# Performance work log

Hardware: AMD Instinct MI355X
Metric: run time of the kernel (lower is better)

## Reference

```python
import jax, jax.numpy as jnp
import numpy as np

N = 100000
E = 1600000
D_IN = 128
D_OUT = 64


def setup_inputs() -> dict:
    key = jax.random.key(0)
    k1, k2, k3, k4, k5 = jax.random.split(key, 5)
    x = jax.random.normal(k1, (N, D_IN), dtype=jnp.float32)
    edge_row = jax.random.randint(k2, (E,), 0, N, dtype=jnp.int32)
    edge_col = jax.random.randint(k3, (E,), 0, N, dtype=jnp.int32)
    edge_val = jax.random.uniform(k4, (E,), dtype=jnp.float32)
    # Glorot-uniform init as in the torch module
    init_range = np.sqrt(6.0 / (D_IN + D_OUT))
    weight = jax.random.uniform(k5, (D_IN, D_OUT), dtype=jnp.float32,
                                minval=-init_range, maxval=init_range)
    return {"x": x, "edge_row": edge_row, "edge_col": edge_col,
            "edge_val": edge_val, "weight": weight}


def reference(x, edge_row, edge_col, edge_val, weight):
    # Dense projection: [N, D_in] @ [D_in, D_out] -> [N, D_out]
    xw = jnp.matmul(x, weight)
    # Sparse aggregation (SpMM with COO support): out[r] += val * xw[c]
    msgs = edge_val[:, None] * xw[edge_col]          # [E, D_out]
    out = jax.ops.segment_sum(msgs, edge_row, num_segments=x.shape[0])
    # bias=False, activation=relu
    return jax.nn.relu(out)
```

## Files before the change

### kernel.cpp

```cpp
#include <hip/hip_runtime.h>

#define NN 100000
#define DIN 128
#define DOUT 64
#define NE 1600000

#define BSHIFT 6
#define BROWS 64
#define NB 1563
#define CAP 1536
#define EPB 8192
#define NBLK 196

#define XWB_B  0u
#define GCUR_B 12800000u
#define BPAD_B (GCUR_B + 8192u)
#define WS_NEED (BPAD_B + (unsigned)NB * CAP * 8u)

typedef unsigned short u16;
typedef unsigned int u32;
typedef __attribute__((ext_vector_type(8))) short v8s;
typedef __attribute__((ext_vector_type(4))) float v4f;

__device__ __forceinline__ float bf2f(u16 u) {
  return __uint_as_float(((u32)u) << 16);
}
__device__ __forceinline__ u16 f2bf(float f) {
  u32 x = __float_as_uint(f);
  u32 r = x + 0x7fffu + ((x >> 16) & 1u);
  return (u16)(r >> 16);
}

__global__ __launch_bounds__(256) void gemm_kernel(
    const float* __restrict__ x, const float* __restrict__ w,
    u16* __restrict__ xwb) {
  __shared__ u16 wlds[16 * 64 * 8];
  const int t = threadIdx.x;
  const int lane = t & 63;
  const int wv = t >> 6;

  #pragma unroll
  for (int pi = 0; pi < 4; ++pi) {
    const int p = t * 4 + pi;
    const int f = p >> 6, lp = p & 63;
    const int kc = f >> 2, nc = f & 3;
    const int kg = lp >> 4, lr = lp & 15;
    const int kbase = kc * 32 + kg * 8;
    u32 pk[4];
    #pragma unroll
    for (int h = 0; h < 4; ++h) {
      const u32 lo = f2bf(w[(kbase + 2 * h)     * DOUT + nc * 16 + lr]);
      const u32 hi = f2bf(w[(kbase + 2 * h + 1) * DOUT + nc * 16 + lr]);
      pk[h] = lo | (hi << 16);
    }
    *reinterpret_cast<uint4*>(&wlds[p * 8]) =
        make_uint4(pk[0], pk[1], pk[2], pk[3]);
  }
  __syncthreads();

  const int row0 = blockIdx.x * 64 + wv * 16;
  if (row0 >= NN) return;
  const int lrow = lane & 15;
  const int lkg  = lane >> 4;

  v8s Bf[4][4];
  #pragma unroll
  for (int kc = 0; kc < 4; ++kc)
    #pragma unroll
    for (int nc = 0; nc < 4; ++nc)
      Bf[kc][nc] = *reinterpret_cast<const v8s*>(
          &wlds[((kc * 4 + nc) * 64 + lane) * 8]);

  const float* xr = x + (size_t)(row0 + lrow) * DIN + lkg * 8;
  float4 xa[4][2];
  #pragma unroll
  for (int kc = 0; kc < 4; ++kc) {
    xa[kc][0] = *reinterpret_cast<const float4*>(xr + kc * 32);
    xa[kc][1] = *reinterpret_cast<const float4*>(xr + kc * 32 + 4);
  }

  v4f acc[4];
  #pragma unroll
  for (int nc = 0; nc < 4; ++nc) acc[nc] = (v4f){0.f, 0.f, 0.f, 0.f};

  #pragma unroll
  for (int kc = 0; kc < 4; ++kc) {
    v8s Af;
    Af[0] = (short)f2bf(xa[kc][0].x);
    Af[1] = (short)f2bf(xa[kc][0].y);
    Af[2] = (short)f2bf(xa[kc][0].z);
    Af[3] = (short)f2bf(xa[kc][0].w);
    Af[4] = (short)f2bf(xa[kc][1].x);
    Af[5] = (short)f2bf(xa[kc][1].y);
    Af[6] = (short)f2bf(xa[kc][1].z);
    Af[7] = (short)f2bf(xa[kc][1].w);
    #pragma unroll
    for (int nc = 0; nc < 4; ++nc)
      acc[nc] = __builtin_amdgcn_mfma_f32_16x16x32_bf16(Af, Bf[kc][nc],
                                                        acc[nc], 0, 0, 0);
  }

  #pragma unroll
  for (int nc = 0; nc < 4; ++nc)
    #pragma unroll
    for (int j = 0; j < 4; ++j)
      xwb[(size_t)(row0 + lkg * 4 + j) * DOUT + nc * 16 + lrow] =
          f2bf(acc[nc][j]);
}

__global__ __launch_bounds__(1024) void place3_kernel(
    const int* __restrict__ erow, const int* __restrict__ ecol,
    const float* __restrict__ eval_, int* __restrict__ gcur,
    int2* __restrict__ bpad) {
  __shared__ int  hist[2048];
  __shared__ int  lofs[NB + 1];
  __shared__ int  lcur[NB];
  __shared__ int  base_[NB];
  __shared__ int  wtot[16];
  __shared__ u16  sb[EPB];
  __shared__ int2 dstl[EPB];

  const int t = threadIdx.x;
  const int lane = t & 63;
  const int wv = t >> 6;
  const int blk = blockIdx.x;
  const int e0 = blk * EPB;
  const int e1 = min(e0 + EPB, NE);
  const int ecount = e1 - e0;

  for (int i = t; i < 2048; i += 1024) hist[i] = 0;
  for (int i = t; i < NB; i += 1024) lcur[i] = 0;
  __syncthreads();

  int er[8];
  #pragma unroll
  for (int k = 0; k < 8; ++k) {
    const int e = e0 + t + k * 1024;
    er[k] = (e < e1) ? erow[e] : -1;
    if (er[k] >= 0) atomicAdd(&hist[er[k] >> BSHIFT], 1);
  }
  __syncthreads();

  const int ha = hist[2 * t], hb = hist[2 * t + 1];
  const int ps = ha + hb;
  int s = ps;
  #pragma unroll
  for (int o = 1; o < 64; o <<= 1) {
    const int u = __shfl_up(s, o);
    if (lane >= o) s += u;
  }
  if (lane == 63) wtot[wv] = s;
  __syncthreads();
  int woff = 0;
  #pragma unroll
  for (int w = 0; w < 16; ++w) woff += (w < wv) ? wtot[w] : 0;
  const int excl = woff + s - ps;
  if (2 * t     <= NB) lofs[2 * t]     = excl;
  if (2 * t + 1 <= NB) lofs[2 * t + 1] = excl + ha;
  for (int i = t; i < NB; i += 1024) {
    const int h = hist[i];
    base_[i] = h ? atomicAdd(&gcur[i], h) : 0;
  }
  __syncthreads();

  #pragma unroll
  for (int k = 0; k < 8; ++k) {
    const int e = e0 + t + k * 1024;
    if (er[k] >= 0) {
      const int b = er[k] >> BSHIFT;
      const int pos = lofs[b] + atomicAdd(&lcur[b], 1);
      int2 q;
      q.x = ((er[k] & (BROWS - 1)) << 17) | ecol[e];
      q.y = __float_as_int(eval_[e]);
      dstl[pos] = q;
      sb[pos] = (u16)b;
    }
  }
  __syncthreads();

  for (int p = t; p < ecount; p += 1024) {
    const int b = sb[p];
    const int rk = base_[b] + (p - lofs[b]);
    if (rk < CAP) bpad[(long)b * CAP + rk] = dstl[p];
  }
}

__global__ __launch_bounds__(256) void agg2_kernel(
    const int* __restrict__ gcur, const int2* __restrict__ bpad,
    const u16* __restrict__ xwb, float* __restrict__ out) {
  __shared__ int2 dst[CAP];
  __shared__ int  hist[BROWS];
  __shared__ int  lptr[BROWS + 1];
  __shared__ int  cur[BROWS];

  const int bucket = blockIdx.x;
  const int t = threadIdx.x;
  const int count = min(gcur[bucket], CAP);
  const long sbase = (long)bucket * CAP;

  if (t < BROWS) hist[t] = 0;
  __syncthreads();

  int2 qr[6];
  #pragma unroll
  for (int k = 0; k < 6; ++k) {
    const int e = t + k * 256;
    if (e < count) {
      qr[k] = bpad[sbase + e];
      atomicAdd(&hist[(qr[k].x >> 17) & (BROWS - 1)], 1);
    }
  }
  __syncthreads();

  if (t < 64) {
    const int v = hist[t];
    int s = v;
    #pragma unroll
    for (int o = 1; o < 64; o <<= 1) {
      const int u = __shfl_up(s, o);
      if (t >= o) s += u;
    }
    lptr[t + 1] = s;
    cur[t] = s - v;
    if (t == 0) lptr[0] = 0;
  }
  __syncthreads();

  #pragma unroll
  for (int k = 0; k < 6; ++k) {
    const int e = t + k * 256;
    if (e < count) {
      const int r = (qr[k].x >> 17) & (BROWS - 1);
      const int pos = atomicAdd(&cur[r], 1);
      dst[pos] = qr[k];
    }
  }
  __syncthreads();

  const int lane = t & 63;
  const int wave = t >> 6;
  const int slot = lane >> 4;
  const int li   = lane & 15;
  const int row0 = bucket << BSHIFT;
  const int cmax = count - 1;

  for (int r = wave; r < BROWS; r += 4) {
    const int row = row0 + r;
    if (row >= NN) break;
    const int s = lptr[r], en = lptr[r + 1];
    float a0 = 0.f, a1 = 0.f, a2 = 0.f, a3 = 0.f;
    for (int e = s; e < en; e += 8) {
      {
        const int idx = e + slot;
        const int2 q = dst[min(idx, cmax)];
        const float v = (idx < en) ? __int_as_float(q.y) : 0.f;
        const u32 col = (u32)q.x & 0x1FFFFu;
        const uint2 g = *reinterpret_cast<const uint2*>(
            xwb + (size_t)col * DOUT + li * 4);
        a0 = fmaf(v, __uint_as_float(g.x << 16), a0);
        a1 = fmaf(v, __uint_as_float(g.x & 0xFFFF0000u), a1);
        a2 = fmaf(v, __uint_as_float(g.y << 16), a2);
        a3 = fmaf(v, __uint_as_float(g.y & 0xFFFF0000u), a3);
      }
      {
        const int idx = e + 4 + slot;
        const int2 q = dst[min(idx, cmax)];
        const float v = (idx < en) ? __int_as_float(q.y) : 0.f;
        const u32 col = (u32)q.x & 0x1FFFFu;
        const uint2 g = *reinterpret_cast<const uint2*>(
            xwb + (size_t)col * DOUT + li * 4);
        a0 = fmaf(v, __uint_as_float(g.x << 16), a0);
        a1 = fmaf(v, __uint_as_float(g.x & 0xFFFF0000u), a1);
        a2 = fmaf(v, __uint_as_float(g.y << 16), a2);
        a3 = fmaf(v, __uint_as_float(g.y & 0xFFFF0000u), a3);
      }
    }
    a0 += __shfl_xor(a0, 16); a0 += __shfl_xor(a0, 32);
    a1 += __shfl_xor(a1, 16); a1 += __shfl_xor(a1, 32);
    a2 += __shfl_xor(a2, 16); a2 += __shfl_xor(a2, 32);
    a3 += __shfl_xor(a3, 16); a3 += __shfl_xor(a3, 32);
    if (slot == 0) {
      float4 o;
      o.x = fmaxf(a0, 0.f); o.y = fmaxf(a1, 0.f);
      o.z = fmaxf(a2, 0.f); o.w = fmaxf(a3, 0.f);
      *reinterpret_cast<float4*>(&out[(size_t)row * DOUT + li * 4]) = o;
    }
  }
}

__global__ __launch_bounds__(256) void scatter_kernel(
    const int* __restrict__ erow, const int* __restrict__ ecol,
    const float* __restrict__ eval_, const u16* __restrict__ xwb,
    float* __restrict__ out) {
  const int wave = (blockIdx.x * blockDim.x + threadIdx.x) >> 6;
  const int lane = threadIdx.x & 63;
  const int nwaves = (gridDim.x * blockDim.x) >> 6;
  const int per = (NE + nwaves - 1) / nwaves;
  const int e0 = wave * per;
  const int e1 = min(e0 + per, NE);
  for (int base = e0; base < e1; base += 64) {
    const int e = base + lane;
    int r = 0, c = 0; float v = 0.f;
    if (e < e1) { r = erow[e]; c = ecol[e]; v = eval_[e]; }
    const int cnt = min(64, e1 - base);
    for (int j = 0; j < cnt; ++j) {
      const int rj = __shfl(r, j);
      const int cj = __shfl(c, j);
      const float vj = __shfl(v, j);
      atomicAdd(&out[rj * DOUT + lane], vj * bf2f(xwb[cj * DOUT + lane]));
    }
  }
}

__global__ __launch_bounds__(256) void finish_kernel(float* __restrict__ out) {
  const int idx = (blockIdx.x * blockDim.x + threadIdx.x) * 4;
  if (idx < NN * DOUT) {
    float4 a = *reinterpret_cast<const float4*>(&out[idx]);
    a.x = fmaxf(a.x, 0.f); a.y = fmaxf(a.y, 0.f);
    a.z = fmaxf(a.z, 0.f); a.w = fmaxf(a.w, 0.f);
    *reinterpret_cast<float4*>(&out[idx]) = a;
  }
}

extern "C" void kernel_launch(void* const* d_in, const int* in_sizes, int n_in,
                              void* d_out, int out_size, void* d_ws, size_t ws_size,
                              hipStream_t stream) {
  const float* x     = (const float*)d_in[0];
  const int*   erow  = (const int*)d_in[1];
  const int*   ecol  = (const int*)d_in[2];
  const float* eval_ = (const float*)d_in[3];
  const float* w     = (const float*)d_in[4];
  float* out = (float*)d_out;

  char* ws = (char*)d_ws;
  u16* xwb = (u16*)(ws + XWB_B);

  const int gemm_grid = (NN + 63) / 64;
  gemm_kernel<<<gemm_grid, 256, 0, stream>>>(x, w, xwb);

  if (ws_size >= (size_t)WS_NEED) {
    int*  gcur = (int*)(ws + GCUR_B);
    int2* bpad = (int2*)(ws + BPAD_B);

    hipMemsetAsync(gcur, 0, NB * 4, stream);
    place3_kernel<<<NBLK, 1024, 0, stream>>>(erow, ecol, eval_, gcur, bpad);
    agg2_kernel<<<NB, 256, 0, stream>>>(gcur, bpad, xwb, out);
  } else {
    hipMemsetAsync(d_out, 0, (size_t)NN * DOUT * sizeof(float), stream);
    scatter_kernel<<<2048, 256, 0, stream>>>(erow, ecol, eval_, xwb, out);
    const int fin_grid = (NN * DOUT / 4 + 255) / 256;
    finish_kernel<<<fin_grid, 256, 0, stream>>>(out);
  }
}
```

Measured before the change: 73.89 us.

## Use 256-row buckets, fold gcur zeroing into GEMM, retune place/agg blocks

Enlarges the row buckets from 64 to 256 rows, cutting the bucket count to 391. The placement kernel now runs 512-thread blocks over 4096 edges each, and the aggregation kernel runs 512 threads per bucket with a larger LDS staging buffer. The separate memset of the bucket counters is removed; the GEMM kernel zeroes them instead, which saves one launch. Risks are lower occupancy from the larger LDS footprint (about 38KB per agg block) and bucket overflow if any bucket exceeds the 4736-edge cap.

```diff
diff --git a/kernel.cpp b/kernel.cpp
--- a/kernel.cpp
+++ b/kernel.cpp
@@ -5,17 +5,17 @@
 #define DOUT 64
 #define NE 1600000
 
-#define BSHIFT 6
-#define BROWS 64
-#define NB 1563
-#define CAP 1536
-#define EPB 8192
-#define NBLK 196
+#define BSHIFT 8
+#define BROWS 256
+#define NBB 391
+#define CAP 4736
+#define EPB 4096
+#define NBLK 391
 
 #define XWB_B  0u
 #define GCUR_B 12800000u
 #define BPAD_B (GCUR_B + 8192u)
-#define WS_NEED (BPAD_B + (unsigned)NB * CAP * 8u)
+#define WS_NEED (BPAD_B + (unsigned)NBB * CAP * 8u)
 
 typedef unsigned short u16;
 typedef unsigned int u32;
@@ -33,7 +33,10 @@
 
 __global__ __launch_bounds__(256) void gemm_kernel(
     const float* __restrict__ x, const float* __restrict__ w,
-    u16* __restrict__ xwb) {
+    u16* __restrict__ xwb, int* __restrict__ gz) {
+  if (gz != nullptr && threadIdx.x == 0 && blockIdx.x < NBB)
+    gz[blockIdx.x] = 0;
+
   __shared__ u16 wlds[16 * 64 * 8];
   const int t = threadIdx.x;
   const int lane = t & 63;
@@ -108,42 +111,47 @@
           f2bf(acc[nc][j]);
 }
 
-__global__ __launch_bounds__(1024) void place3_kernel(
+__global__ __launch_bounds__(512) void place4_kernel(
     const int* __restrict__ erow, const int* __restrict__ ecol,
     const float* __restrict__ eval_, int* __restrict__ gcur,
     int2* __restrict__ bpad) {
-  __shared__ int  hist[2048];
-  __shared__ int  lofs[NB + 1];
-  __shared__ int  lcur[NB];
-  __shared__ int  base_[NB];
-  __shared__ int  wtot[16];
+  __shared__ int  hist[512];
+  __shared__ int  lofs[512];
+  __shared__ int  lcur[512];
+  __shared__ int  base_[512];
+  __shared__ int  wtot[8];
   __shared__ u16  sb[EPB];
   __shared__ int2 dstl[EPB];
 
   const int t = threadIdx.x;
   const int lane = t & 63;
   const int wv = t >> 6;
-  const int blk = blockIdx.x;
-  const int e0 = blk * EPB;
+  const int e0 = blockIdx.x * EPB;
   const int e1 = min(e0 + EPB, NE);
   const int ecount = e1 - e0;
 
-  for (int i = t; i < 2048; i += 1024) hist[i] = 0;
-  for (int i = t; i < NB; i += 1024) lcur[i] = 0;
-  __syncthreads();
-
-  int er[8];
+  hist[t] = 0;
+  lcur[t] = 0;
+  __syncthreads();
+
+  int er[8], ec[8];
+  float ev[8];
   #pragma unroll
   for (int k = 0; k < 8; ++k) {
-    const int e = e0 + t + k * 1024;
-    er[k] = (e < e1) ? erow[e] : -1;
-    if (er[k] >= 0) atomicAdd(&hist[er[k] >> BSHIFT], 1);
-  }
-  __syncthreads();
-
-  const int ha = hist[2 * t], hb = hist[2 * t + 1];
-  const int ps = ha + hb;
-  int s = ps;
+    const int e = e0 + t + k * 512;
+    if (e < e1) {
+      er[k] = erow[e];
+      ec[k] = ecol[e];
+      ev[k] = eval_[e];
+      atomicAdd(&hist[er[k] >> BSHIFT], 1);
+    } else {
+      er[k] = -1;
+    }
+  }
+  __syncthreads();
+
+  const int h = hist[t];
+  int s = h;
   #pragma unroll
   for (int o = 1; o < 64; o <<= 1) {
     const int u = __shfl_up(s, o);
@@ -153,39 +161,31 @@
   __syncthreads();
   int woff = 0;
   #pragma unroll
-  for (int w = 0; w < 16; ++w) woff += (w < wv) ? wtot[w] : 0;
-  const int excl = woff + s - ps;
-  if (2 * t     <= NB) lofs[2 * t]     = excl;
-  if (2 * t + 1 <= NB) lofs[2 * t + 1] = excl + ha;
-  for (int i = t; i < NB; i += 1024) {
-    const int h = hist[i];
-    base_[i] = h ? atomicAdd(&gcur[i], h) : 0;
-  }
+  for (int w = 0; w < 8; ++w) woff += (w < wv) ? wtot[w] : 0;
+  lofs[t] = woff + s - h;
+  base_[t] = (h && t < NBB) ? atomicAdd(&gcur[t], h) : 0;
   __syncthreads();
 
   #pragma unroll
   for (int k = 0; k < 8; ++k) {
-    const int e = e0 + t + k * 1024;
     if (er[k] >= 0) {
       const int b = er[k] >> BSHIFT;
       const int pos = lofs[b] + atomicAdd(&lcur[b], 1);
-      int2 q;
-      q.x = ((er[k] & (BROWS - 1)) << 17) | ecol[e];
-      q.y = __float_as_int(eval_[e]);
-      dstl[pos] = q;
+      dstl[pos] = make_int2(((er[k] & (BROWS - 1)) << 17) | ec[k],
+                            __float_as_int(ev[k]));
       sb[pos] = (u16)b;
     }
   }
   __syncthreads();
 
-  for (int p = t; p < ecount; p += 1024) {
+  for (int p = t; p < ecount; p += 512) {
     const int b = sb[p];
     const int rk = base_[b] + (p - lofs[b]);
     if (rk < CAP) bpad[(long)b * CAP + rk] = dstl[p];
   }
 }
 
-__global__ __launch_bounds__(256) void agg2_kernel(
+__global__ __launch_bounds__(512) void agg5_kernel(
     const int* __restrict__ gcur, const int2* __restrict__ bpad,
     const u16* __restrict__ xwb, float* __restrict__ out) {
   __shared__ int2 dst[CAP];
@@ -201,39 +201,34 @@
   if (t < BROWS) hist[t] = 0;
   __syncthreads();
 
-  int2 qr[6];
-  #pragma unroll
-  for (int k = 0; k < 6; ++k) {
-    const int e = t + k * 256;
-    if (e < count) {
-      qr[k] = bpad[sbase + e];
-      atomicAdd(&hist[(qr[k].x >> 17) & (BROWS - 1)], 1);
-    }
-  }
+  for (int e = t; e < count; e += 512)
+    atomicAdd(&hist[(bpad[sbase + e].x >> 17) & (BROWS - 1)], 1);
   __syncthreads();
 
   if (t < 64) {
-    const int v = hist[t];
-    int s = v;
+    const int h0 = hist[4 * t],     h1 = hist[4 * t + 1];
+    const int h2 = hist[4 * t + 2], h3 = hist[4 * t + 3];
+    const int ps = h0 + h1 + h2 + h3;
+    int s = ps;
     #pragma unroll
     for (int o = 1; o < 64; o <<= 1) {
       const int u = __shfl_up(s, o);
       if (t >= o) s += u;
     }
-    lptr[t + 1] = s;
-    cur[t] = s - v;
-    if (t == 0) lptr[0] = 0;
-  }
-  __syncthreads();
-
-  #pragma unroll
-  for (int k = 0; k < 6; ++k) {
-    const int e = t + k * 256;
-    if (e < count) {
-      const int r = (qr[k].x >> 17) & (BROWS - 1);
-      const int pos = atomicAdd(&cur[r], 1);
-      dst[pos] = qr[k];
-    }
+    const int excl = s - ps;
+    lptr[4 * t]     = excl;                cur[4 * t]     = excl;
+    lptr[4 * t + 1] = excl + h0;           cur[4 * t + 1] = excl + h0;
+    lptr[4 * t + 2] = excl + h0 + h1;      cur[4 * t + 2] = excl + h0 + h1;
+    lptr[4 * t + 3] = excl + h0 + h1 + h2; cur[4 * t + 3] = excl + h0 + h1 + h2;
+    if (t == 63) lptr[BROWS] = s;
+  }
+  __syncthreads();
+
+  for (int e = t; e < count; e += 512) {
+    const int2 q = bpad[sbase + e];
+    const int r = (q.x >> 17) & (BROWS - 1);
+    const int pos = atomicAdd(&cur[r], 1);
+    dst[pos] = q;
   }
   __syncthreads();
 
@@ -244,7 +239,7 @@
   const int row0 = bucket << BSHIFT;
   const int cmax = count - 1;
 
-  for (int r = wave; r < BROWS; r += 4) {
+  for (int r = wave; r < BROWS; r += 8) {
     const int row = row0 + r;
     if (row >= NN) break;
     const int s = lptr[r], en = lptr[r + 1];
@@ -334,17 +329,16 @@
 
   char* ws = (char*)d_ws;
   u16* xwb = (u16*)(ws + XWB_B);
+  const bool big_ws = (ws_size >= (size_t)WS_NEED);
+  int* gcur = big_ws ? (int*)(ws + GCUR_B) : nullptr;
 
   const int gemm_grid = (NN + 63) / 64;
-  gemm_kernel<<<gemm_grid, 256, 0, stream>>>(x, w, xwb);
-
-  if (ws_size >= (size_t)WS_NEED) {
-    int*  gcur = (int*)(ws + GCUR_B);
+  gemm_kernel<<<gemm_grid, 256, 0, stream>>>(x, w, xwb, gcur);
+
+  if (big_ws) {
     int2* bpad = (int2*)(ws + BPAD_B);
-
-    hipMemsetAsync(gcur, 0, NB * 4, stream);
-    place3_kernel<<<NBLK, 1024, 0, stream>>>(erow, ecol, eval_, gcur, bpad);
-    agg2_kernel<<<NB, 256, 0, stream>>>(gcur, bpad, xwb, out);
+    place4_kernel<<<NBLK, 512, 0, stream>>>(erow, ecol, eval_, gcur, bpad);
+    agg5_kernel<<<NBB, 512, 0, stream>>>(gcur, bpad, xwb, out);
   } else {
     hipMemsetAsync(d_out, 0, (size_t)NN * DOUT * sizeof(float), stream);
     scatter_kernel<<<2048, 256, 0, stream>>>(erow, ecol, eval_, xwb, out);
```

Measured after the change: 89.94 us. +21.7%, slower.
